# Optimization experiments

Hardware: AMD Instinct MI355X
Metric: run time of the kernel (lower is better)

The kernel has to match this reference:

```python
import math
import jax, jax.numpy as jnp
import numpy as np

NUM_GROUPS = 32
EPS = 1e-5


def setup_inputs() -> dict:
    key = jax.random.key(0)
    ks = jax.random.split(key, 4)
    b, c, h, w = 8, 512, 64, 64
    x = jax.random.normal(ks[0], (b, c, h, w), dtype=jnp.float32)
    norm_w = jnp.ones((c,), jnp.float32)
    norm_b = jnp.zeros((c,), jnp.float32)
    qkv_w = jax.random.normal(ks[1], (3 * c, c), dtype=jnp.float32) * (1.0 / math.sqrt(c))
    qkv_b = jnp.zeros((3 * c,), jnp.float32)
    out_w = jax.random.normal(ks[2], (c, c), dtype=jnp.float32) * (1.0 / math.sqrt(c))
    out_b = jnp.zeros((c,), jnp.float32)
    return {"x": x, "norm_w": norm_w, "norm_b": norm_b, "qkv_w": qkv_w,
            "qkv_b": qkv_b, "out_w": out_w, "out_b": out_b}


def reference(x, norm_w, norm_b, qkv_w, qkv_b, out_w, out_b):
    b, c, h, w = x.shape
    L = h * w
    # GroupNorm over (c/g, h, w) per group
    xg = x.reshape(b, NUM_GROUPS, -1)
    mu = xg.mean(axis=-1, keepdims=True)
    var = xg.var(axis=-1, keepdims=True)
    xn = ((xg - mu) * jax.lax.rsqrt(var + EPS)).reshape(b, c, L)
    xn = xn * norm_w[:, None] + norm_b[:, None]
    # 1x1 conv == channel matmul -> qkv [b, 3c, L]
    qkv = jnp.einsum('oc,bcl->bol', qkv_w, xn) + qkv_b[:, None]
    q, k, v = jnp.split(qkv, 3, axis=1)  # each [b, c, L]
    scale = 1.0 / math.sqrt(c)
    attn = jax.nn.softmax(jnp.einsum('bcl,bcs->bls', q, k) * scale, axis=-1)
    o = jnp.einsum('bls,bcs->bcl', attn, v)  # [b, c, L]
    o = jnp.einsum('oc,bcl->bol', out_w, o) + out_b[:, None]
    return o.reshape(b, c, h, w) + x
```

## Files before the change

### kernel.cpp

```cpp
#include <hip/hip_runtime.h>
#include <cstdint>

static constexpr int B_ = 8, C_ = 512, L_ = 4096, NG_ = 32;
static constexpr float RSCALE = 0.04419417382415922f;
static constexpr float RSCALE_LOG2E = 0.0637587149159965f;

using f32x4  = __attribute__((ext_vector_type(4))) float;
using bf16x8 = __attribute__((ext_vector_type(8))) short;

__device__ __forceinline__ uint16_t f2bf(float f) {
  union { float f; uint32_t u; } v{f};
  uint32_t r = (v.u + 0x7fffu + ((v.u >> 16) & 1u)) >> 16;
  return (uint16_t)r;
}

__device__ __forceinline__ void gll16(const uint16_t* g, uint16_t* l) {
  __builtin_amdgcn_global_load_lds((const __attribute__((address_space(1))) uint32_t*)g,
                                   (__attribute__((address_space(3))) uint32_t*)l,
                                   16, 0, 0);
}

__device__ __forceinline__ void bar_lgkm() {
  asm volatile("s_waitcnt lgkmcnt(0)" ::: "memory");
  __builtin_amdgcn_s_barrier();
  asm volatile("" ::: "memory");
}
__device__ __forceinline__ void bar_vm_lgkm() {
  asm volatile("s_waitcnt vmcnt(0) lgkmcnt(0)" ::: "memory");
  __builtin_amdgcn_s_barrier();
  asm volatile("" ::: "memory");
}

__global__ __launch_bounds__(256) void k_cvt_bf16(const float* __restrict__ in,
                                                  uint16_t* __restrict__ out, int n) {
  int i = (blockIdx.x * 256 + threadIdx.x) * 4;
  if (i + 3 < n) {
    float4 v = *(const float4*)(in + i);
    union { uint16_t s[4]; uint2 u; } o;
    o.s[0] = f2bf(v.x); o.s[1] = f2bf(v.y); o.s[2] = f2bf(v.z); o.s[3] = f2bf(v.w);
    *(uint2*)(out + i) = o.u;
  }
}

__global__ __launch_bounds__(256) void k_gnstats(const float* __restrict__ x,
                                                 float* __restrict__ mu, float* __restrict__ rs) {
  int bg = blockIdx.x;
  const float* p = x + (size_t)bg * (16 * L_);
  float s = 0.f, s2 = 0.f;
#pragma unroll 8
  for (int i = 0; i < 64; ++i) {
    float4 v = *(const float4*)(p + (threadIdx.x + i * 256) * 4);
    s  += v.x + v.y + v.z + v.w;
    s2 += v.x * v.x + v.y * v.y + v.z * v.z + v.w * v.w;
  }
  for (int o = 32; o; o >>= 1) { s += __shfl_down(s, o); s2 += __shfl_down(s2, o); }
  __shared__ float as_[4], as2_[4];
  int w = threadIdx.x >> 6;
  if ((threadIdx.x & 63) == 0) { as_[w] = s; as2_[w] = s2; }
  __syncthreads();
  if (threadIdx.x == 0) {
    float S = as_[0] + as_[1] + as_[2] + as_[3];
    float S2 = as2_[0] + as2_[1] + as2_[2] + as2_[3];
    float m = S / 65536.0f;
    float var = S2 / 65536.0f - m * m;
    mu[bg] = m; rs[bg] = rsqrtf(var + 1e-5f);
  }
}

__global__ __launch_bounds__(256) void k_normT(const float* __restrict__ x,
                                               const float* __restrict__ nw, const float* __restrict__ nb,
                                               const float* __restrict__ mu, const float* __restrict__ rs,
                                               uint16_t* __restrict__ xnT) {
  __shared__ __align__(16) uint16_t t[64][72];
  int l0 = blockIdx.x * 64, c0 = blockIdx.y * 64, b = blockIdx.z;
#pragma unroll
  for (int i = 0; i < 4; ++i) {
    int idx = threadIdx.x + i * 256;
    int row = idx >> 4, q = idx & 15;
    int c = c0 + row;
    float m_ = mu[b * NG_ + (c >> 4)], r_ = rs[b * NG_ + (c >> 4)];
    float sc = r_ * nw[c], sh = nb[c] - m_ * sc;
    float4 v = *(const float4*)(x + (size_t)(b * C_ + c) * L_ + l0 + q * 4);
    int lb = q * 4;
    t[lb + 0][row] = f2bf(v.x * sc + sh);
    t[lb + 1][row] = f2bf(v.y * sc + sh);
    t[lb + 2][row] = f2bf(v.z * sc + sh);
    t[lb + 3][row] = f2bf(v.w * sc + sh);
  }
  __syncthreads();
#pragma unroll
  for (int i = 0; i < 2; ++i) {
    int idx = threadIdx.x + i * 256;
    int row = idx >> 3, ch = idx & 7;
    uint4 v = *(const uint4*)(&t[row][ch * 8]);
    *(uint4*)(xnT + (size_t)(b * L_ + l0 + row) * C_ + c0 + ch * 8) = v;
  }
}

__global__ __launch_bounds__(256) void k_vT(const uint16_t* __restrict__ qkvT, uint16_t* __restrict__ vn) {
  __shared__ __align__(16) uint16_t t[64][72];
  int l0 = blockIdx.x * 64, c0 = blockIdx.y * 64, b = blockIdx.z;
#pragma unroll
  for (int i = 0; i < 2; ++i) {
    int idx = threadIdx.x + i * 256;
    int row = idx >> 3, ch = idx & 7;
    uint16_t v[8];
    *(uint4*)v = *(const uint4*)(qkvT + (size_t)(b * L_ + l0 + row) * 1536 + 1024 + c0 + ch * 8);
#pragma unroll
    for (int j = 0; j < 8; ++j) t[ch * 8 + j][row] = v[j];
  }
  __syncthreads();
#pragma unroll
  for (int i = 0; i < 2; ++i) {
    int idx = threadIdx.x + i * 256;
    int row = idx >> 3, ch = idx & 7;
    *(uint4*)(vn + (size_t)(b * C_ + c0 + row) * L_ + l0 + ch * 8) = *(const uint4*)(&t[row][ch * 8]);
  }
}

template <int MODE>
__global__ __launch_bounds__(256, 2) void k_gemm(const uint16_t* __restrict__ Ag, int lda, long long strideA,
                                                 const uint16_t* __restrict__ Bg, int ldb, long long strideB,
                                                 void* __restrict__ Cg, long long strideC,
                                                 const float* __restrict__ bias,
                                                 const float* __restrict__ resid) {
  __shared__ __align__(16) uint16_t Asm[128 * 64], Bsm[128 * 64];
  int b = blockIdx.z;
  int m0 = blockIdx.y * 128, n0 = blockIdx.x * 128;
  const uint16_t* A = Ag + (size_t)b * strideA;
  const uint16_t* Bp = Bg + (size_t)b * strideB;
  int lane = threadIdx.x & 63, w = threadIdx.x >> 6;
  int wm = w >> 1, wn = w & 1;
  int l15 = lane & 15, lhi = lane >> 4;
  f32x4 acc[4][4] = {};
  for (int kt = 0; kt < 512; kt += 64) {
#pragma unroll
    for (int i = 0; i < 4; ++i) {
      int idx = threadIdx.x + i * 256;
      int row = idx >> 3, cs = idx & 7, cg = cs ^ (row & 7);
      *(uint4*)(Asm + row * 64 + cs * 8) = *(const uint4*)(A + (size_t)(m0 + row) * lda + kt + cg * 8);
      *(uint4*)(Bsm + row * 64 + cs * 8) = *(const uint4*)(Bp + (size_t)(n0 + row) * ldb + kt + cg * 8);
    }
    __syncthreads();
#pragma unroll
    for (int kk = 0; kk < 2; ++kk) {
      bf16x8 af[4], bfr[4];
      int chunk = kk * 4 + lhi;
#pragma unroll
      for (int m = 0; m < 4; ++m) {
        int row = wm * 64 + m * 16 + l15;
        af[m] = *(const bf16x8*)(Asm + row * 64 + ((chunk ^ (row & 7)) << 3));
      }
#pragma unroll
      for (int n = 0; n < 4; ++n) {
        int row = wn * 64 + n * 16 + l15;
        bfr[n] = *(const bf16x8*)(Bsm + row * 64 + ((chunk ^ (row & 7)) << 3));
      }
#pragma unroll
      for (int m = 0; m < 4; ++m)
#pragma unroll
        for (int n = 0; n < 4; ++n)
          acc[m][n] = __builtin_amdgcn_mfma_f32_16x16x32_bf16(af[m], bfr[n], acc[m][n], 0, 0, 0);
    }
    __syncthreads();
  }
  if (MODE == 0) {
    uint16_t* Cp = (uint16_t*)Cg + (size_t)b * strideC;
#pragma unroll
    for (int n = 0; n < 4; ++n) {
      int col = n0 + wn * 64 + n * 16 + l15;
      float bs = bias[col];
      float scl = (col < 512) ? RSCALE_LOG2E : 1.0f;
#pragma unroll
      for (int m = 0; m < 4; ++m) {
        int rowb = m0 + wm * 64 + m * 16 + lhi * 4;
#pragma unroll
        for (int r = 0; r < 4; ++r)
          Cp[(size_t)(rowb + r) * 1536 + col] = f2bf((acc[m][n][r] + bs) * scl);
      }
    }
  } else {
    float* Cp = (float*)Cg + (size_t)b * strideC;
    const float* Xp = resid + (size_t)b * strideC;
#pragma unroll
    for (int m = 0; m < 4; ++m) {
      int rowb = m0 + wm * 64 + m * 16 + lhi * 4;
#pragma unroll
      for (int n = 0; n < 4; ++n) {
        int col = n0 + wn * 64 + n * 16 + l15;
#pragma unroll
        for (int r = 0; r < 4; ++r) {
          float v = acc[m][n][r] + bias[rowb + r] + Xp[(size_t)(rowb + r) * 4096 + col];
          Cp[(size_t)(rowb + r) * 4096 + col] = v;
        }
      }
    }
  }
}

__global__ __launch_bounds__(512, 2) void k_attn(const uint16_t* __restrict__ qkvT,
                                                 const uint16_t* __restrict__ vn,
                                                 uint16_t* __restrict__ ot) {
  __shared__ __align__(16) uint16_t kbuf[2][64 * 512];
  __shared__ __align__(16) uint16_t ps[64 * 64];
  __shared__ __align__(16) float lsh[2][64];

  const int tid = threadIdx.x, lane = tid & 63, w = tid >> 6;
  const int l15 = lane & 15, lhi = lane >> 4;
  const int b = blockIdx.x & 7, q0 = (blockIdx.x >> 3) * 64;
  const int nf = w & 3, mh = w >> 2;
  const int s3 = l15 & 7;

  const uint16_t* kg = qkvT + (size_t)b * L_ * 1536 + 512;
  const uint16_t* vg = vn + (size_t)b * C_ * L_ + (size_t)(w * 64) * L_;

  const int cswz  = (lhi ^ s3) << 3;
  const int off00 = (mh * 32 + l15) * 512 + cswz;
  const int off10 = (mh * 32 + 16 + l15) * 512 + cswz;
  const int lrow  = nf * 16 + l15;
  const int psw0 = lrow * 64 + ((((mh * 2 + 0) * 2 + (lhi >> 1)) ^ s3) << 3) + (lhi & 1) * 4;
  const int psw1 = lrow * 64 + ((((mh * 2 + 1) * 2 + (lhi >> 1)) ^ s3) << 3) + (lhi & 1) * 4;
  int pab[4];
#pragma unroll
  for (int m = 0; m < 4; ++m) pab[m] = (m * 16 + l15) * 64 + cswz;

  bf16x8 qr[16];
  {
    const uint16_t* qrow = qkvT + (size_t)(b * L_ + q0 + lrow) * 1536 + lhi * 8;
#pragma unroll
    for (int kc = 0; kc < 16; ++kc) qr[kc] = *(const bf16x8*)(qrow + kc * 32);
  }

  const int lswz = lane << 3;
#pragma unroll
  for (int i = 0; i < 8; ++i) {
    int row = w * 8 + i;
    gll16(kg + (size_t)row * 1536 + (lswz ^ (i * 8)), &kbuf[0][row * 512]);
  }

  float lrun = 0.0f;
  f32x4 acc[4][4] = {};
  bar_vm_lgkm();

  for (int st = 0; st < 64; ++st) {
    const uint16_t* kc0 = kbuf[st & 1];
    uint16_t* knxt = kbuf[(st + 1) & 1];

    f32x4 sfr0 = {}, sfr1 = {};
    const bf16x8* a00 = (const bf16x8*)(kc0 + off00);
    const bf16x8* a01 = (const bf16x8*)(kc0 + (off00 ^ 32));
    const bf16x8* a10 = (const bf16x8*)(kc0 + off10);
    const bf16x8* a11 = (const bf16x8*)(kc0 + (off10 ^ 32));
#pragma unroll
    for (int kc2 = 0; kc2 < 8; ++kc2) {
      sfr0 = __builtin_amdgcn_mfma_f32_16x16x32_bf16(a00[kc2 * 8], qr[kc2 * 2], sfr0, 0, 0, 0);
      sfr1 = __builtin_amdgcn_mfma_f32_16x16x32_bf16(a10[kc2 * 8], qr[kc2 * 2], sfr1, 0, 0, 0);
      sfr0 = __builtin_amdgcn_mfma_f32_16x16x32_bf16(a01[kc2 * 8], qr[kc2 * 2 + 1], sfr0, 0, 0, 0);
      sfr1 = __builtin_amdgcn_mfma_f32_16x16x32_bf16(a11[kc2 * 8], qr[kc2 * 2 + 1], sfr1, 0, 0, 0);
    }

    bf16x8 vb[2][4];
    {
      const uint16_t* vrow = vg + st * 64 + lhi * 8;
#pragma unroll
      for (int n = 0; n < 4; ++n) {
        vb[0][n] = *(const bf16x8*)(vrow + (size_t)(n * 16 + l15) * L_);
        vb[1][n] = *(const bf16x8*)(vrow + (size_t)(n * 16 + l15) * L_ + 32);
      }
    }

    float p0[4], p1[4], psum = 0.f;
#pragma unroll
    for (int r = 0; r < 4; ++r) {
      p0[r] = exp2f(sfr0[r]); p1[r] = exp2f(sfr1[r]);
      psum += p0[r] + p1[r];
    }
    psum += __shfl_xor(psum, 16);
    psum += __shfl_xor(psum, 32);
    lrun += psum;

    union { uint16_t h[4]; uint2 u; } pk0, pk1;
#pragma unroll
    for (int r = 0; r < 4; ++r) { pk0.h[r] = f2bf(p0[r]); pk1.h[r] = f2bf(p1[r]); }
    *(uint2*)(ps + psw0) = pk0.u;
    *(uint2*)(ps + psw1) = pk1.u;

    if (st < 63) {
      const uint16_t* kst = kg + (size_t)(st + 1) * 98304 + (size_t)(w * 8) * 1536;
#pragma unroll
      for (int i = 0; i < 8; ++i)
        gll16(kst + (size_t)i * 1536 + (lswz ^ (i * 8)), &knxt[(w * 8 + i) * 512]);
    }

    bar_lgkm();

#pragma unroll
    for (int kk = 0; kk < 2; ++kk) {
      bf16x8 pa[4];
#pragma unroll
      for (int m = 0; m < 4; ++m) pa[m] = *(const bf16x8*)(ps + (pab[m] ^ (kk * 32)));
#pragma unroll
      for (int m = 0; m < 4; ++m)
#pragma unroll
        for (int n = 0; n < 4; ++n)
          acc[m][n] = __builtin_amdgcn_mfma_f32_16x16x32_bf16(pa[m], vb[kk][n], acc[m][n], 0, 0, 0);
    }

    bar_vm_lgkm();
  }

  if (lhi == 0) lsh[mh][lrow] = lrun;
  __syncthreads();
#pragma unroll
  for (int m = 0; m < 4; ++m) {
    f32x4 s0v = *(const f32x4*)(&lsh[0][m * 16 + lhi * 4]);
    f32x4 s1v = *(const f32x4*)(&lsh[1][m * 16 + lhi * 4]);
    f32x4 inv;
#pragma unroll
    for (int r = 0; r < 4; ++r) inv[r] = 1.0f / (s0v[r] + s1v[r]);
#pragma unroll
    for (int n = 0; n < 4; ++n) {
      int c = w * 64 + n * 16 + l15;
#pragma unroll
      for (int r = 0; r < 4; ++r) {
        int l = q0 + m * 16 + lhi * 4 + r;
        ot[(size_t)(b * L_ + l) * C_ + c] = f2bf(acc[m][n][r] * inv[r]);
      }
    }
  }
}

extern "C" void kernel_launch(void* const* d_in, const int* in_sizes, int n_in,
                              void* d_out, int out_size, void* d_ws, size_t ws_size,
                              hipStream_t stream) {
  const float* x  = (const float*)d_in[0];
  const float* nw = (const float*)d_in[1];
  const float* nb = (const float*)d_in[2];
  const float* qw = (const float*)d_in[3];
  const float* qb = (const float*)d_in[4];
  const float* ow = (const float*)d_in[5];
  const float* ob = (const float*)d_in[6];
  float* out = (float*)d_out;
  char* ws = (char*)d_ws;

  float*    mu   = (float*)(ws + 0);
  float*    rs   = (float*)(ws + 1024);
  uint16_t* wq   = (uint16_t*)(ws + 4096);
  uint16_t* wo   = (uint16_t*)(ws + 4096 + 1572864);
  uint16_t* xnT  = (uint16_t*)(ws + 2101248);
  uint16_t* qkvT = (uint16_t*)(ws + 35655680);
  uint16_t* vn   = (uint16_t*)(ws + 136318976);
  uint16_t* otb  = (uint16_t*)(ws + 169873408);

  k_cvt_bf16<<<dim3((1536 * 512) / 1024), 256, 0, stream>>>(qw, wq, 1536 * 512);
  k_cvt_bf16<<<dim3((512 * 512) / 1024), 256, 0, stream>>>(ow, wo, 512 * 512);
  k_gnstats<<<dim3(256), 256, 0, stream>>>(x, mu, rs);
  k_normT<<<dim3(64, 8, 8), 256, 0, stream>>>(x, nw, nb, mu, rs, xnT);
  k_gemm<0><<<dim3(12, 32, 8), 256, 0, stream>>>(xnT, 512, (long long)4096 * 512,
                                                 wq, 512, 0LL,
                                                 qkvT, (long long)4096 * 1536, qb, nullptr);
  k_vT<<<dim3(64, 8, 8), 256, 0, stream>>>(qkvT, vn);
  k_attn<<<dim3(512), 512, 0, stream>>>(qkvT, vn, otb);
  k_gemm<1><<<dim3(32, 4, 8), 256, 0, stream>>>(wo, 512, 0LL,
                                                otb, 512, (long long)4096 * 512,
                                                out, (long long)512 * 4096, ob, x);
}
```

Baseline: 620.6 us.

## Fuse V transpose into QKV GEMM epilogue and rework attention S-tile wave split

The QKV GEMM epilogue now writes the V columns straight into the channel-major vn buffer, which removes the separate k_vT transpose kernel and its extra round trip through global memory. In the attention kernel, each wave now computes S for one 16-key slice across two 16-query row groups, so each K fragment read from LDS feeds two MFMAs. Each wave keeps two Q register sets and two running row sums, and the final normalisation sums four partial sums instead of two. The second half of the V fragments is now loaded after the barrier, which shortens register lifetimes but raises Q register pressure and makes the V epilogue store 8-byte strided pieces.

```diff
diff --git a/kernel.cpp b/kernel.cpp
--- a/kernel.cpp
+++ b/kernel.cpp
@@ -97,33 +97,13 @@
   }
 }
 
-__global__ __launch_bounds__(256) void k_vT(const uint16_t* __restrict__ qkvT, uint16_t* __restrict__ vn) {
-  __shared__ __align__(16) uint16_t t[64][72];
-  int l0 = blockIdx.x * 64, c0 = blockIdx.y * 64, b = blockIdx.z;
-#pragma unroll
-  for (int i = 0; i < 2; ++i) {
-    int idx = threadIdx.x + i * 256;
-    int row = idx >> 3, ch = idx & 7;
-    uint16_t v[8];
-    *(uint4*)v = *(const uint4*)(qkvT + (size_t)(b * L_ + l0 + row) * 1536 + 1024 + c0 + ch * 8);
-#pragma unroll
-    for (int j = 0; j < 8; ++j) t[ch * 8 + j][row] = v[j];
-  }
-  __syncthreads();
-#pragma unroll
-  for (int i = 0; i < 2; ++i) {
-    int idx = threadIdx.x + i * 256;
-    int row = idx >> 3, ch = idx & 7;
-    *(uint4*)(vn + (size_t)(b * C_ + c0 + row) * L_ + l0 + ch * 8) = *(const uint4*)(&t[row][ch * 8]);
-  }
-}
-
 template <int MODE>
 __global__ __launch_bounds__(256, 2) void k_gemm(const uint16_t* __restrict__ Ag, int lda, long long strideA,
                                                  const uint16_t* __restrict__ Bg, int ldb, long long strideB,
                                                  void* __restrict__ Cg, long long strideC,
                                                  const float* __restrict__ bias,
-                                                 const float* __restrict__ resid) {
+                                                 const float* __restrict__ resid,
+                                                 uint16_t* __restrict__ vout) {
   __shared__ __align__(16) uint16_t Asm[128 * 64], Bsm[128 * 64];
   int b = blockIdx.z;
   int m0 = blockIdx.y * 128, n0 = blockIdx.x * 128;
@@ -165,18 +145,37 @@
     __syncthreads();
   }
   if (MODE == 0) {
-    uint16_t* Cp = (uint16_t*)Cg + (size_t)b * strideC;
-#pragma unroll
-    for (int n = 0; n < 4; ++n) {
-      int col = n0 + wn * 64 + n * 16 + l15;
-      float bs = bias[col];
-      float scl = (col < 512) ? RSCALE_LOG2E : 1.0f;
-#pragma unroll
-      for (int m = 0; m < 4; ++m) {
-        int rowb = m0 + wm * 64 + m * 16 + lhi * 4;
-#pragma unroll
-        for (int r = 0; r < 4; ++r)
-          Cp[(size_t)(rowb + r) * 1536 + col] = f2bf((acc[m][n][r] + bs) * scl);
+    const bool isV = (n0 >= 1024);
+    if (!isV) {
+      uint16_t* Cp = (uint16_t*)Cg + (size_t)b * strideC;
+#pragma unroll
+      for (int n = 0; n < 4; ++n) {
+        int col = n0 + wn * 64 + n * 16 + l15;
+        float bs = bias[col];
+        float scl = (col < 512) ? RSCALE_LOG2E : 1.0f;
+#pragma unroll
+        for (int m = 0; m < 4; ++m) {
+          int rowb = m0 + wm * 64 + m * 16 + lhi * 4;
+#pragma unroll
+          for (int r = 0; r < 4; ++r)
+            Cp[(size_t)(rowb + r) * 1536 + col] = f2bf((acc[m][n][r] + bs) * scl);
+        }
+      }
+    } else {
+      uint16_t* Vp = vout + (size_t)b * (C_ * (size_t)L_);
+#pragma unroll
+      for (int n = 0; n < 4; ++n) {
+        int col = n0 + wn * 64 + n * 16 + l15;
+        float bs = bias[col];
+        uint16_t* vc = Vp + (size_t)(col - 1024) * L_;
+#pragma unroll
+        for (int m = 0; m < 4; ++m) {
+          int rowb = m0 + wm * 64 + m * 16 + lhi * 4;
+          union { uint16_t h[4]; uint2 u; } pk;
+#pragma unroll
+          for (int r = 0; r < 4; ++r) pk.h[r] = f2bf(acc[m][n][r] + bs);
+          *(uint2*)(vc + rowb) = pk.u;
+        }
       }
     }
   } else {
@@ -203,32 +202,35 @@
                                                  uint16_t* __restrict__ ot) {
   __shared__ __align__(16) uint16_t kbuf[2][64 * 512];
   __shared__ __align__(16) uint16_t ps[64 * 64];
-  __shared__ __align__(16) float lsh[2][64];
+  __shared__ __align__(16) float lsh[4][64];
 
   const int tid = threadIdx.x, lane = tid & 63, w = tid >> 6;
   const int l15 = lane & 15, lhi = lane >> 4;
   const int b = blockIdx.x & 7, q0 = (blockIdx.x >> 3) * 64;
-  const int nf = w & 3, mh = w >> 2;
+  const int sf = w >> 1, lfp = w & 1;
   const int s3 = l15 & 7;
 
   const uint16_t* kg = qkvT + (size_t)b * L_ * 1536 + 512;
   const uint16_t* vg = vn + (size_t)b * C_ * L_ + (size_t)(w * 64) * L_;
 
-  const int cswz  = (lhi ^ s3) << 3;
-  const int off00 = (mh * 32 + l15) * 512 + cswz;
-  const int off10 = (mh * 32 + 16 + l15) * 512 + cswz;
-  const int lrow  = nf * 16 + l15;
-  const int psw0 = lrow * 64 + ((((mh * 2 + 0) * 2 + (lhi >> 1)) ^ s3) << 3) + (lhi & 1) * 4;
-  const int psw1 = lrow * 64 + ((((mh * 2 + 1) * 2 + (lhi >> 1)) ^ s3) << 3) + (lhi & 1) * 4;
+  const int cswz = (lhi ^ s3) << 3;
+  const int offK = (sf * 16 + l15) * 512 + cswz;
+  const int pch  = ((((sf << 1) | (lhi >> 1)) ^ s3) << 3) + (lhi & 1) * 4;
+  const int psw0 = (lfp * 32 + l15) * 64 + pch;
+  const int psw1 = psw0 + 16 * 64;
   int pab[4];
 #pragma unroll
   for (int m = 0; m < 4; ++m) pab[m] = (m * 16 + l15) * 64 + cswz;
 
-  bf16x8 qr[16];
+  bf16x8 qr0[16], qr1[16];
   {
-    const uint16_t* qrow = qkvT + (size_t)(b * L_ + q0 + lrow) * 1536 + lhi * 8;
-#pragma unroll
-    for (int kc = 0; kc < 16; ++kc) qr[kc] = *(const bf16x8*)(qrow + kc * 32);
+    const uint16_t* qp0 = qkvT + (size_t)(b * L_ + q0 + lfp * 32 + l15) * 1536 + lhi * 8;
+    const uint16_t* qp1 = qp0 + 16 * 1536;
+#pragma unroll
+    for (int kc = 0; kc < 16; ++kc) {
+      qr0[kc] = *(const bf16x8*)(qp0 + kc * 32);
+      qr1[kc] = *(const bf16x8*)(qp1 + kc * 32);
+    }
   }
 
   const int lswz = lane << 3;
@@ -238,7 +240,7 @@
     gll16(kg + (size_t)row * 1536 + (lswz ^ (i * 8)), &kbuf[0][row * 512]);
   }
 
-  float lrun = 0.0f;
+  float lrun0 = 0.0f, lrun1 = 0.0f;
   f32x4 acc[4][4] = {};
   bar_vm_lgkm();
 
@@ -247,37 +249,34 @@
     uint16_t* knxt = kbuf[(st + 1) & 1];
 
     f32x4 sfr0 = {}, sfr1 = {};
-    const bf16x8* a00 = (const bf16x8*)(kc0 + off00);
-    const bf16x8* a01 = (const bf16x8*)(kc0 + (off00 ^ 32));
-    const bf16x8* a10 = (const bf16x8*)(kc0 + off10);
-    const bf16x8* a11 = (const bf16x8*)(kc0 + (off10 ^ 32));
+    const bf16x8* aK0 = (const bf16x8*)(kc0 + offK);
+    const bf16x8* aK1 = (const bf16x8*)(kc0 + (offK ^ 32));
 #pragma unroll
     for (int kc2 = 0; kc2 < 8; ++kc2) {
-      sfr0 = __builtin_amdgcn_mfma_f32_16x16x32_bf16(a00[kc2 * 8], qr[kc2 * 2], sfr0, 0, 0, 0);
-      sfr1 = __builtin_amdgcn_mfma_f32_16x16x32_bf16(a10[kc2 * 8], qr[kc2 * 2], sfr1, 0, 0, 0);
-      sfr0 = __builtin_amdgcn_mfma_f32_16x16x32_bf16(a01[kc2 * 8], qr[kc2 * 2 + 1], sfr0, 0, 0, 0);
-      sfr1 = __builtin_amdgcn_mfma_f32_16x16x32_bf16(a11[kc2 * 8], qr[kc2 * 2 + 1], sfr1, 0, 0, 0);
-    }
-
-    bf16x8 vb[2][4];
+      bf16x8 ak0 = aK0[kc2 * 8];
+      sfr0 = __builtin_amdgcn_mfma_f32_16x16x32_bf16(ak0, qr0[kc2 * 2], sfr0, 0, 0, 0);
+      sfr1 = __builtin_amdgcn_mfma_f32_16x16x32_bf16(ak0, qr1[kc2 * 2], sfr1, 0, 0, 0);
+      bf16x8 ak1 = aK1[kc2 * 8];
+      sfr0 = __builtin_amdgcn_mfma_f32_16x16x32_bf16(ak1, qr0[kc2 * 2 + 1], sfr0, 0, 0, 0);
+      sfr1 = __builtin_amdgcn_mfma_f32_16x16x32_bf16(ak1, qr1[kc2 * 2 + 1], sfr1, 0, 0, 0);
+    }
+
+    bf16x8 vb0[4];
     {
       const uint16_t* vrow = vg + st * 64 + lhi * 8;
 #pragma unroll
-      for (int n = 0; n < 4; ++n) {
-        vb[0][n] = *(const bf16x8*)(vrow + (size_t)(n * 16 + l15) * L_);
-        vb[1][n] = *(const bf16x8*)(vrow + (size_t)(n * 16 + l15) * L_ + 32);
-      }
-    }
-
-    float p0[4], p1[4], psum = 0.f;
+      for (int n = 0; n < 4; ++n) vb0[n] = *(const bf16x8*)(vrow + (size_t)(n * 16 + l15) * L_);
+    }
+
+    float p0[4], p1[4], ps0 = 0.f, ps1 = 0.f;
 #pragma unroll
     for (int r = 0; r < 4; ++r) {
       p0[r] = exp2f(sfr0[r]); p1[r] = exp2f(sfr1[r]);
-      psum += p0[r] + p1[r];
-    }
-    psum += __shfl_xor(psum, 16);
-    psum += __shfl_xor(psum, 32);
-    lrun += psum;
+      ps0 += p0[r]; ps1 += p1[r];
+    }
+    ps0 += __shfl_xor(ps0, 16); ps0 += __shfl_xor(ps0, 32);
+    ps1 += __shfl_xor(ps1, 16); ps1 += __shfl_xor(ps1, 32);
+    lrun0 += ps0; lrun1 += ps1;
 
     union { uint16_t h[4]; uint2 u; } pk0, pk1;
 #pragma unroll
@@ -294,30 +293,51 @@
 
     bar_lgkm();
 
-#pragma unroll
-    for (int kk = 0; kk < 2; ++kk) {
+    bf16x8 vb1[4];
+    {
+      const uint16_t* vrow = vg + st * 64 + 32 + lhi * 8;
+#pragma unroll
+      for (int n = 0; n < 4; ++n) vb1[n] = *(const bf16x8*)(vrow + (size_t)(n * 16 + l15) * L_);
+    }
+
+    {
       bf16x8 pa[4];
 #pragma unroll
-      for (int m = 0; m < 4; ++m) pa[m] = *(const bf16x8*)(ps + (pab[m] ^ (kk * 32)));
+      for (int m = 0; m < 4; ++m) pa[m] = *(const bf16x8*)(ps + pab[m]);
 #pragma unroll
       for (int m = 0; m < 4; ++m)
 #pragma unroll
         for (int n = 0; n < 4; ++n)
-          acc[m][n] = __builtin_amdgcn_mfma_f32_16x16x32_bf16(pa[m], vb[kk][n], acc[m][n], 0, 0, 0);
+          acc[m][n] = __builtin_amdgcn_mfma_f32_16x16x32_bf16(pa[m], vb0[n], acc[m][n], 0, 0, 0);
+    }
+    {
+      bf16x8 pa[4];
+#pragma unroll
+      for (int m = 0; m < 4; ++m) pa[m] = *(const bf16x8*)(ps + (pab[m] ^ 32));
+#pragma unroll
+      for (int m = 0; m < 4; ++m)
+#pragma unroll
+        for (int n = 0; n < 4; ++n)
+          acc[m][n] = __builtin_amdgcn_mfma_f32_16x16x32_bf16(pa[m], vb1[n], acc[m][n], 0, 0, 0);
     }
 
     bar_vm_lgkm();
   }
 
-  if (lhi == 0) lsh[mh][lrow] = lrun;
+  if (lhi == 0) {
+    lsh[sf][lfp * 32 + l15] = lrun0;
+    lsh[sf][lfp * 32 + 16 + l15] = lrun1;
+  }
   __syncthreads();
 #pragma unroll
   for (int m = 0; m < 4; ++m) {
     f32x4 s0v = *(const f32x4*)(&lsh[0][m * 16 + lhi * 4]);
     f32x4 s1v = *(const f32x4*)(&lsh[1][m * 16 + lhi * 4]);
+    f32x4 s2v = *(const f32x4*)(&lsh[2][m * 16 + lhi * 4]);
+    f32x4 s3v = *(const f32x4*)(&lsh[3][m * 16 + lhi * 4]);
     f32x4 inv;
 #pragma unroll
-    for (int r = 0; r < 4; ++r) inv[r] = 1.0f / (s0v[r] + s1v[r]);
+    for (int r = 0; r < 4; ++r) inv[r] = 1.0f / (s0v[r] + s1v[r] + s2v[r] + s3v[r]);
 #pragma unroll
     for (int n = 0; n < 4; ++n) {
       int c = w * 64 + n * 16 + l15;
@@ -358,10 +378,9 @@
   k_normT<<<dim3(64, 8, 8), 256, 0, stream>>>(x, nw, nb, mu, rs, xnT);
   k_gemm<0><<<dim3(12, 32, 8), 256, 0, stream>>>(xnT, 512, (long long)4096 * 512,
                                                  wq, 512, 0LL,
-                                                 qkvT, (long long)4096 * 1536, qb, nullptr);
-  k_vT<<<dim3(64, 8, 8), 256, 0, stream>>>(qkvT, vn);
+                                                 qkvT, (long long)4096 * 1536, qb, nullptr, vn);
   k_attn<<<dim3(512), 512, 0, stream>>>(qkvT, vn, otb);
   k_gemm<1><<<dim3(32, 4, 8), 256, 0, stream>>>(wo, 512, 0LL,
                                                 otb, 512, (long long)4096 * 512,
-                                                out, (long long)512 * 4096, ob, x);
-}
+                                                out, (long long)512 * 4096, ob, x, nullptr);
+}
```

Result: slower. 660.9 us (+6.5%).

## Fuse V transpose into QKV GEMM epilogue and single-buffer K in attention

Applied to the files above, without the earlier changes.

The QKV GEMM epilogue now writes the V part directly in channel-major layout, so the separate k_vT transpose kernel and its extra global round trip are removed. The attention kernel drops K double buffering and uses one 64KB LDS buffer. The next K tile is loaded after the barrier that follows the QK^T reads, and the launch bounds rise to 4 blocks per SM for higher occupancy. The cost is that K loads no longer overlap the QK^T phase as fully, and the strided V stores in the GEMM epilogue are less coalesced.

```diff
diff --git a/kernel.cpp b/kernel.cpp
--- a/kernel.cpp
+++ b/kernel.cpp
@@ -97,33 +97,13 @@
   }
 }
 
-__global__ __launch_bounds__(256) void k_vT(const uint16_t* __restrict__ qkvT, uint16_t* __restrict__ vn) {
-  __shared__ __align__(16) uint16_t t[64][72];
-  int l0 = blockIdx.x * 64, c0 = blockIdx.y * 64, b = blockIdx.z;
-#pragma unroll
-  for (int i = 0; i < 2; ++i) {
-    int idx = threadIdx.x + i * 256;
-    int row = idx >> 3, ch = idx & 7;
-    uint16_t v[8];
-    *(uint4*)v = *(const uint4*)(qkvT + (size_t)(b * L_ + l0 + row) * 1536 + 1024 + c0 + ch * 8);
-#pragma unroll
-    for (int j = 0; j < 8; ++j) t[ch * 8 + j][row] = v[j];
-  }
-  __syncthreads();
-#pragma unroll
-  for (int i = 0; i < 2; ++i) {
-    int idx = threadIdx.x + i * 256;
-    int row = idx >> 3, ch = idx & 7;
-    *(uint4*)(vn + (size_t)(b * C_ + c0 + row) * L_ + l0 + ch * 8) = *(const uint4*)(&t[row][ch * 8]);
-  }
-}
-
 template <int MODE>
 __global__ __launch_bounds__(256, 2) void k_gemm(const uint16_t* __restrict__ Ag, int lda, long long strideA,
                                                  const uint16_t* __restrict__ Bg, int ldb, long long strideB,
                                                  void* __restrict__ Cg, long long strideC,
                                                  const float* __restrict__ bias,
-                                                 const float* __restrict__ resid) {
+                                                 const float* __restrict__ resid,
+                                                 uint16_t* __restrict__ vout) {
   __shared__ __align__(16) uint16_t Asm[128 * 64], Bsm[128 * 64];
   int b = blockIdx.z;
   int m0 = blockIdx.y * 128, n0 = blockIdx.x * 128;
@@ -165,18 +145,37 @@
     __syncthreads();
   }
   if (MODE == 0) {
-    uint16_t* Cp = (uint16_t*)Cg + (size_t)b * strideC;
-#pragma unroll
-    for (int n = 0; n < 4; ++n) {
-      int col = n0 + wn * 64 + n * 16 + l15;
-      float bs = bias[col];
-      float scl = (col < 512) ? RSCALE_LOG2E : 1.0f;
-#pragma unroll
-      for (int m = 0; m < 4; ++m) {
-        int rowb = m0 + wm * 64 + m * 16 + lhi * 4;
-#pragma unroll
-        for (int r = 0; r < 4; ++r)
-          Cp[(size_t)(rowb + r) * 1536 + col] = f2bf((acc[m][n][r] + bs) * scl);
+    const bool isV = (n0 >= 1024);
+    if (!isV) {
+      uint16_t* Cp = (uint16_t*)Cg + (size_t)b * strideC;
+#pragma unroll
+      for (int n = 0; n < 4; ++n) {
+        int col = n0 + wn * 64 + n * 16 + l15;
+        float bs = bias[col];
+        float scl = (col < 512) ? RSCALE_LOG2E : 1.0f;
+#pragma unroll
+        for (int m = 0; m < 4; ++m) {
+          int rowb = m0 + wm * 64 + m * 16 + lhi * 4;
+#pragma unroll
+          for (int r = 0; r < 4; ++r)
+            Cp[(size_t)(rowb + r) * 1536 + col] = f2bf((acc[m][n][r] + bs) * scl);
+        }
+      }
+    } else {
+      uint16_t* Vp = vout + (size_t)b * (C_ * (size_t)L_);
+#pragma unroll
+      for (int n = 0; n < 4; ++n) {
+        int col = n0 + wn * 64 + n * 16 + l15;
+        float bs = bias[col];
+        uint16_t* vc = Vp + (size_t)(col - 1024) * L_;
+#pragma unroll
+        for (int m = 0; m < 4; ++m) {
+          int rowb = m0 + wm * 64 + m * 16 + lhi * 4;
+          union { uint16_t h[4]; uint2 u; } pk;
+#pragma unroll
+          for (int r = 0; r < 4; ++r) pk.h[r] = f2bf(acc[m][n][r] + bs);
+          *(uint2*)(vc + rowb) = pk.u;
+        }
       }
     }
   } else {
@@ -198,10 +197,11 @@
   }
 }
 
-__global__ __launch_bounds__(512, 2) void k_attn(const uint16_t* __restrict__ qkvT,
-                                                 const uint16_t* __restrict__ vn,
-                                                 uint16_t* __restrict__ ot) {
-  __shared__ __align__(16) uint16_t kbuf[2][64 * 512];
+__global__ __launch_bounds__(512, 4)
+void k_attn(const uint16_t* __restrict__ qkvT,
+            const uint16_t* __restrict__ vn,
+            uint16_t* __restrict__ ot) {
+  __shared__ __align__(16) uint16_t kbuf[64 * 512];
   __shared__ __align__(16) uint16_t ps[64 * 64];
   __shared__ __align__(16) float lsh[2][64];
 
@@ -235,22 +235,20 @@
 #pragma unroll
   for (int i = 0; i < 8; ++i) {
     int row = w * 8 + i;
-    gll16(kg + (size_t)row * 1536 + (lswz ^ (i * 8)), &kbuf[0][row * 512]);
+    gll16(kg + (size_t)row * 1536 + (lswz ^ (i * 8)), &kbuf[row * 512]);
   }
 
   float lrun = 0.0f;
   f32x4 acc[4][4] = {};
-  bar_vm_lgkm();
 
   for (int st = 0; st < 64; ++st) {
-    const uint16_t* kc0 = kbuf[st & 1];
-    uint16_t* knxt = kbuf[(st + 1) & 1];
+    bar_vm_lgkm();
 
     f32x4 sfr0 = {}, sfr1 = {};
-    const bf16x8* a00 = (const bf16x8*)(kc0 + off00);
-    const bf16x8* a01 = (const bf16x8*)(kc0 + (off00 ^ 32));
-    const bf16x8* a10 = (const bf16x8*)(kc0 + off10);
-    const bf16x8* a11 = (const bf16x8*)(kc0 + (off10 ^ 32));
+    const bf16x8* a00 = (const bf16x8*)(kbuf + off00);
+    const bf16x8* a01 = (const bf16x8*)(kbuf + (off00 ^ 32));
+    const bf16x8* a10 = (const bf16x8*)(kbuf + off10);
+    const bf16x8* a11 = (const bf16x8*)(kbuf + (off10 ^ 32));
 #pragma unroll
     for (int kc2 = 0; kc2 < 8; ++kc2) {
       sfr0 = __builtin_amdgcn_mfma_f32_16x16x32_bf16(a00[kc2 * 8], qr[kc2 * 2], sfr0, 0, 0, 0);
@@ -285,14 +283,15 @@
     *(uint2*)(ps + psw0) = pk0.u;
     *(uint2*)(ps + psw1) = pk1.u;
 
-    if (st < 63) {
-      const uint16_t* kst = kg + (size_t)(st + 1) * 98304 + (size_t)(w * 8) * 1536;
+    bar_lgkm();
+
+    {
+      const int stn = (st + 1) & 63;
+      const uint16_t* kst = kg + (size_t)stn * 98304 + (size_t)(w * 8) * 1536;
 #pragma unroll
       for (int i = 0; i < 8; ++i)
-        gll16(kst + (size_t)i * 1536 + (lswz ^ (i * 8)), &knxt[(w * 8 + i) * 512]);
-    }
-
-    bar_lgkm();
+        gll16(kst + (size_t)i * 1536 + (lswz ^ (i * 8)), &kbuf[(w * 8 + i) * 512]);
+    }
 
 #pragma unroll
     for (int kk = 0; kk < 2; ++kk) {
@@ -305,8 +304,6 @@
         for (int n = 0; n < 4; ++n)
           acc[m][n] = __builtin_amdgcn_mfma_f32_16x16x32_bf16(pa[m], vb[kk][n], acc[m][n], 0, 0, 0);
     }
-
-    bar_vm_lgkm();
   }
 
   if (lhi == 0) lsh[mh][lrow] = lrun;
@@ -358,10 +355,9 @@
   k_normT<<<dim3(64, 8, 8), 256, 0, stream>>>(x, nw, nb, mu, rs, xnT);
   k_gemm<0><<<dim3(12, 32, 8), 256, 0, stream>>>(xnT, 512, (long long)4096 * 512,
                                                  wq, 512, 0LL,
-                                                 qkvT, (long long)4096 * 1536, qb, nullptr);
-  k_vT<<<dim3(64, 8, 8), 256, 0, stream>>>(qkvT, vn);
+                                                 qkvT, (long long)4096 * 1536, qb, nullptr, vn);
   k_attn<<<dim3(512), 512, 0, stream>>>(qkvT, vn, otb);
   k_gemm<1><<<dim3(32, 4, 8), 256, 0, stream>>>(wo, 512, 0LL,
                                                 otb, 512, (long long)4096 * 512,
-                                                out, (long long)512 * 4096, ob, x);
-}
+                                                out, (long long)512 * 4096, ob, x, nullptr);
+}
```

After: 1.116 ms. +79.8%, slower.
